# Optimization experiments

Hardware: AMD Instinct MI355X
Metric: run time of the kernel (lower is better)

The kernel has to match this reference:

```python
import jax, jax.numpy as jnp
import numpy as np

NUM_HEADS = 12
HEAD_DIM = 64
HIDDEN = 768
QMAX = 127.0  # 8-bit symmetric
DOMAIN_MIN, DOMAIN_MAX = -10.0, 0.0
NUM_INTERVALS = 12


def _build_pla_coeffs():
    xs = np.linspace(DOMAIN_MIN, DOMAIN_MAX, 1001)
    ys = np.exp(xs)
    intervals = np.linspace(DOMAIN_MIN, DOMAIN_MAX, NUM_INTERVALS + 1)
    ms, cs = [], []
    for i in range(NUM_INTERVALS):
        a, b = intervals[i], intervals[i + 1]
        mask = (xs >= a) & (xs <= b)
        m, c = np.polyfit(xs[mask], ys[mask], 1)
        ms.append(m)
        cs.append(c)
    return (jnp.asarray(ms, jnp.float32), jnp.asarray(cs, jnp.float32),
            jnp.asarray(intervals, jnp.float32))

COEFFS_M, COEFFS_C, INTERVALS = _build_pla_coeffs()


def quantize(x):
    # per-row (last-dim) abs-max symmetric 8-bit fake quant
    max_val = jnp.max(jnp.abs(x), axis=-1, keepdims=True)
    scale = max_val / QMAX
    scale = jnp.where(scale == 0, 1.0, scale)
    return jnp.clip(jnp.round(x / scale), -QMAX, QMAX) * scale


def to_fixed_point(x, bits=32, frac_bits=26):
    scale = 2.0 ** frac_bits
    lo = -2.0 ** (bits - 1)
    hi = 2.0 ** (bits - 1) - 1
    return jnp.clip(jnp.round(x * scale), lo, hi) / scale


def pla_exp(x):
    xc = jnp.clip(x, DOMAIN_MIN, DOMAIN_MAX)
    # sum(x >= intervals) - 1 == searchsorted(intervals, x, 'right') - 1
    idx = jnp.clip(jnp.searchsorted(INTERVALS, xc, side='right') - 1, 0, NUM_INTERVALS - 1)
    return COEFFS_M[idx] * xc + COEFFS_C[idx]


def pla_softmax(scores):
    shifted = scores - jnp.max(scores, axis=-1, keepdims=True)
    shifted_fx = to_fixed_point(shifted, 32, 26)
    exps = pla_exp(shifted_fx)
    sm = exps / (jnp.sum(exps, axis=-1, keepdims=True) + 1e-9)
    return quantize(sm)


def q_linear(x, W, b):
    # QuantizedLinear: quantize input and weight (per-row), fp bias
    return quantize(x) @ quantize(W).T + b


def split_heads(x):
    B, S, _ = x.shape
    return x.reshape(B, S, NUM_HEADS, HEAD_DIM).transpose(0, 2, 1, 3)  # bhsd


def mhsa(hidden_states, Wq, bq, Wk, bk, Wv, bv, Wo, bo):
    B, S, H = hidden_states.shape
    scale = HEAD_DIM ** -0.5
    q = split_heads(q_linear(hidden_states, Wq, bq))
    k = split_heads(q_linear(hidden_states, Wk, bk))
    v = split_heads(q_linear(hidden_states, Wv, bv))
    # per-row quantization makes tile-wise quant identical to full quant
    scores = jnp.einsum('bhqd,bhkd->bhqk', quantize(q), quantize(k)) * scale
    probs = pla_softmax(scores)
    ctx = jnp.einsum('bhqk,bhkd->bhqd', probs, quantize(v))
    ctx = ctx.transpose(0, 2, 1, 3).reshape(B, S, H)
    return q_linear(ctx, Wo, bo)


def setup_inputs() -> dict:
    key = jax.random.key(0)
    ks = jax.random.split(key, 9)
    B, S = 8, 512
    hs = jax.random.normal(ks[0], (B, S, HIDDEN), dtype=jnp.float32)
    def w(k):
        return jax.random.normal(k, (HIDDEN, HIDDEN), dtype=jnp.float32) * 0.02
    def b(k):
        return jax.random.normal(k, (HIDDEN,), dtype=jnp.float32) * 0.02
    return {
        'hidden_states': hs,
        'Wq': w(ks[1]), 'bq': b(ks[2]),
        'Wk': w(ks[3]), 'bk': b(ks[4]),
        'Wv': w(ks[5]), 'bv': b(ks[6]),
        'Wo': w(ks[7]), 'bo': b(ks[8]),
    }


def reference(hidden_states, Wq, bq, Wk, bk, Wv, bv, Wo, bo):
    return mhsa(hidden_states, Wq, bq, Wk, bk, Wv, bv, Wo, bo)
```

## Files before the change

### kernel.cpp

```cpp
#include <hip/hip_runtime.h>
#include <cmath>

#define R_TOT 4096
#define HID   768
#define NHEAD 12
#define HDIM  64
#define SEQ   512
#define BATCH 8

typedef int   v4i  __attribute__((ext_vector_type(4)));
typedef float v4f  __attribute__((ext_vector_type(4)));
typedef _Float16 half8 __attribute__((ext_vector_type(8)));
typedef _Float16 half4v __attribute__((ext_vector_type(4)));

struct PlaConsts { float m[12]; float c[12]; float b[13]; };

static PlaConsts build_pla() {
  PlaConsts pc;
  const int NPTS = 1001;
  static double xs[NPTS], ys[NPTS];
  const double step = 10.0 / 1000.0;
  for (int j = 0; j < NPTS; ++j) xs[j] = (double)j * step + (-10.0);
  xs[NPTS - 1] = 0.0;
  for (int j = 0; j < NPTS; ++j) ys[j] = std::exp(xs[j]);
  double bnd[13];
  const double step2 = 10.0 / 12.0;
  for (int k = 0; k < 13; ++k) bnd[k] = (double)k * step2 + (-10.0);
  bnd[12] = 0.0;
  for (int i = 0; i < 12; ++i) {
    const double a = bnd[i], bb = bnd[i + 1];
    double sx = 0, sy = 0; int n = 0;
    for (int j = 0; j < NPTS; ++j)
      if (xs[j] >= a && xs[j] <= bb) { sx += xs[j]; sy += ys[j]; ++n; }
    const double xm = sx / n, ym = sy / n;
    double sxx = 0, sxy = 0;
    for (int j = 0; j < NPTS; ++j)
      if (xs[j] >= a && xs[j] <= bb) {
        const double dx = xs[j] - xm;
        sxx += dx * dx; sxy += dx * (ys[j] - ym);
      }
    const double m = sxy / sxx;
    pc.m[i] = (float)m;
    pc.c[i] = (float)(ym - m * xm);
  }
  for (int k = 0; k < 13; ++k) pc.b[k] = (float)bnd[k];
  return pc;
}
static const PlaConsts g_pla = build_pla();

__device__ __forceinline__ void quant_row_body(const float* __restrict__ x,
                                               signed char* __restrict__ qrow,
                                               float* __restrict__ srow) {
  const float v0 = x[threadIdx.x];
  const float v1 = x[threadIdx.x + 256];
  const float v2 = x[threadIdx.x + 512];
  float m = fmaxf(fmaxf(fabsf(v0), fabsf(v1)), fabsf(v2));
  #pragma unroll
  for (int off = 32; off; off >>= 1) m = fmaxf(m, __shfl_xor(m, off));
  __shared__ float red[4];
  const int lane = threadIdx.x & 63, wv = threadIdx.x >> 6;
  if (lane == 0) red[wv] = m;
  __syncthreads();
  if (threadIdx.x == 0) {
    float mm = fmaxf(fmaxf(red[0], red[1]), fmaxf(red[2], red[3]));
    float s = mm / 127.0f;
    if (s == 0.f) s = 1.f;
    red[0] = s;
    *srow = s;
  }
  __syncthreads();
  const float s = red[0];
  qrow[threadIdx.x] =
      (signed char)(int)fminf(fmaxf(rintf(v0 / s), -127.f), 127.f);
  qrow[threadIdx.x + 256] =
      (signed char)(int)fminf(fmaxf(rintf(v1 / s), -127.f), 127.f);
  qrow[threadIdx.x + 512] =
      (signed char)(int)fminf(fmaxf(rintf(v2 / s), -127.f), 127.f);
}

__global__ __launch_bounds__(256)
void quant_rows(const float* __restrict__ src,
                signed char* __restrict__ qout, float* __restrict__ sout) {
  const int row = blockIdx.x;
  quant_row_body(src + (size_t)row * HID, qout + (size_t)row * HID, sout + row);
}

__global__ __launch_bounds__(256)
void quant_all(const float* hs, const float* w0, const float* w1,
               const float* w2, const float* w3,
               signed char* qx, float* sx,
               signed char* q0, signed char* q1, signed char* q2, signed char* q3,
               float* s0, float* s1, float* s2, float* s3) {
  const int bid = blockIdx.x;
  const float* src; signed char* qo; float* so; int row;
  if (bid < R_TOT)            { src = hs; qo = qx; so = sx; row = bid; }
  else if (bid < R_TOT + 768) { src = w0; qo = q0; so = s0; row = bid - R_TOT; }
  else if (bid < R_TOT + 1536){ src = w1; qo = q1; so = s1; row = bid - R_TOT - 768; }
  else if (bid < R_TOT + 2304){ src = w2; qo = q2; so = s2; row = bid - R_TOT - 1536; }
  else                        { src = w3; qo = q3; so = s3; row = bid - R_TOT - 2304; }
  quant_row_body(src + (size_t)row * HID, qo + (size_t)row * HID, so + row);
}

__device__ __forceinline__
void proj_body(int mode,
               const signed char* __restrict__ qx, const float* __restrict__ sx,
               const signed char* __restrict__ qw, const float* __restrict__ sw,
               const float* __restrict__ bias,
               signed char* __restrict__ qo, float* __restrict__ so,
               _Float16* __restrict__ vt, float* __restrict__ fo,
               signed char* Al, signed char* Bl) {
  const int tid = threadIdx.x;
  const int w = tid >> 6, lane = tid & 63;
  const int n = lane & 15, quad = lane >> 4;
  const int row0 = blockIdx.x * 128, col0 = blockIdx.y * 64;
  const int ar = tid >> 1, ac = (tid & 1) * 64;
  const int br = tid >> 2, bc = (tid & 3) * 32;
  v4i acc[2][4];
  #pragma unroll
  for (int s = 0; s < 2; ++s)
    #pragma unroll
    for (int j = 0; j < 4; ++j) acc[s][j] = (v4i){0, 0, 0, 0};
  for (int k0 = 0; k0 < HID; k0 += 128) {
    const signed char* ap = qx + (size_t)(row0 + ar) * HID + k0 + ac;
    const int4 a0 = *(const int4*)(ap);
    const int4 a1 = *(const int4*)(ap + 16);
    const int4 a2 = *(const int4*)(ap + 32);
    const int4 a3 = *(const int4*)(ap + 48);
    const signed char* bp = qw + (size_t)(col0 + br) * HID + k0 + bc;
    const int4 b0 = *(const int4*)(bp);
    const int4 b1 = *(const int4*)(bp + 16);
    if (k0) __syncthreads();
    *(int4*)&Al[ar * 144 + ac]      = a0;
    *(int4*)&Al[ar * 144 + ac + 16] = a1;
    *(int4*)&Al[ar * 144 + ac + 32] = a2;
    *(int4*)&Al[ar * 144 + ac + 48] = a3;
    *(int4*)&Bl[br * 144 + bc]      = b0;
    *(int4*)&Bl[br * 144 + bc + 16] = b1;
    __syncthreads();
    #pragma unroll
    for (int ks = 0; ks < 128; ks += 64) {
      const v4i af0 = *(const v4i*)&Al[(w * 16 + n) * 144 + ks + quad * 16];
      const v4i af1 = *(const v4i*)&Al[(64 + w * 16 + n) * 144 + ks + quad * 16];
      #pragma unroll
      for (int j = 0; j < 4; ++j) {
        const v4i bf = *(const v4i*)&Bl[(j * 16 + n) * 144 + ks + quad * 16];
        acc[0][j] = __builtin_amdgcn_mfma_i32_16x16x64_i8(af0, bf, acc[0][j], 0, 0, 0);
        acc[1][j] = __builtin_amdgcn_mfma_i32_16x16x64_i8(af1, bf, acc[1][j], 0, 0, 0);
      }
    }
  }
  float swc4[4], bc4[4];
  #pragma unroll
  for (int j = 0; j < 4; ++j) {
    swc4[j] = sw[col0 + j * 16 + n];
    bc4[j] = bias[col0 + j * 16 + n];
  }
  #pragma unroll
  for (int s = 0; s < 2; ++s) {
    const int mrow = s * 64 + w * 16 + quad * 4;
    float sxr[4];
    #pragma unroll
    for (int r = 0; r < 4; ++r) sxr[r] = sx[row0 + mrow + r];
    float vals[4][4];
    #pragma unroll
    for (int j = 0; j < 4; ++j)
      #pragma unroll
      for (int r = 0; r < 4; ++r)
        vals[j][r] = (float)acc[s][j][r] * (sxr[r] * swc4[j]) + bc4[j];
    if (mode == 1) {
      const int h = blockIdx.y;
      #pragma unroll
      for (int r = 0; r < 4; ++r) {
        float m = 0.f;
        #pragma unroll
        for (int j = 0; j < 4; ++j) m = fmaxf(m, fabsf(vals[j][r]));
        #pragma unroll
        for (int off = 1; off < 16; off <<= 1) m = fmaxf(m, __shfl_xor(m, off));
        float sq = m / 127.0f;
        if (sq == 0.f) sq = 1.f;
        const int grow = row0 + mrow + r;
        const int bidx = grow >> 9, sidx = grow & 511;
        const size_t rowidx = ((size_t)bidx * NHEAD + h) * SEQ + sidx;
        #pragma unroll
        for (int j = 0; j < 4; ++j) {
          float q = fminf(fmaxf(rintf(vals[j][r] / sq), -127.f), 127.f);
          qo[rowidx * HDIM + j * 16 + n] = (signed char)(int)q;
        }
        if (n == 0) so[rowidx] = sq;
      }
    } else if (mode == 2) {
      const int h = blockIdx.y;
      float srow[4];
      #pragma unroll
      for (int r = 0; r < 4; ++r) {
        float m = 0.f;
        #pragma unroll
        for (int j = 0; j < 4; ++j) m = fmaxf(m, fabsf(vals[j][r]));
        #pragma unroll
        for (int off = 1; off < 16; off <<= 1) m = fmaxf(m, __shfl_xor(m, off));
        float sq = m / 127.0f;
        if (sq == 0.f) sq = 1.f;
        srow[r] = sq;
      }
      const int grow0 = row0 + mrow;
      const int bidx = grow0 >> 9, sidx = grow0 & 511;
      const int kb = sidx >> 5, ko = sidx & 31;
      const size_t hbv = (size_t)bidx * NHEAD + h;
      #pragma unroll
      for (int j = 0; j < 4; ++j) {
        half4v hv;
        #pragma unroll
        for (int r = 0; r < 4; ++r) {
          float q = fminf(fmaxf(rintf(vals[j][r] / srow[r]), -127.f), 127.f);
          hv[r] = (_Float16)(q * srow[r]);
        }
        *(half4v*)(vt + ((hbv * 16 + kb) * 64 + j * 16 + n) * 32 + ko) = hv;
      }
    } else {
      #pragma unroll
      for (int r = 0; r < 4; ++r) {
        const size_t base = (size_t)(row0 + mrow + r) * HID + col0;
        #pragma unroll
        for (int j = 0; j < 4; ++j)
          fo[base + j * 16 + n] = vals[j][r];
      }
    }
  }
}

__global__ __launch_bounds__(256)
void proj_qkv(const signed char* __restrict__ qx, const float* __restrict__ sx,
              const signed char* qwq, const float* swq, const float* bq,
              signed char* qqd, float* qqs,
              const signed char* qwk, const float* swk, const float* bk,
              signed char* qkd, float* qks,
              const signed char* qwv, const float* swv, const float* bv,
              _Float16* vt2) {
  __shared__ __align__(16) signed char Al[128 * 144];
  __shared__ __align__(16) signed char Bl[64 * 144];
  if (blockIdx.z == 0)
    proj_body(1, qx, sx, qwq, swq, bq, qqd, qqs, nullptr, nullptr, Al, Bl);
  else if (blockIdx.z == 1)
    proj_body(1, qx, sx, qwk, swk, bk, qkd, qks, nullptr, nullptr, Al, Bl);
  else
    proj_body(2, qx, sx, qwv, swv, bv, nullptr, nullptr, vt2, nullptr, Al, Bl);
}

__global__ __launch_bounds__(256)
void proj_out(const signed char* __restrict__ qx, const float* __restrict__ sx,
              const signed char* qw, const float* sw, const float* bias,
              float* fo) {
  __shared__ __align__(16) signed char Al[128 * 144];
  __shared__ __align__(16) signed char Bl[64 * 144];
  proj_body(0, qx, sx, qw, sw, bias, nullptr, nullptr, nullptr, fo, Al, Bl);
}

__device__ __forceinline__
void softmax_exp_tile(float (&s)[8][4], float mx26, const float4* __restrict__ pt4,
                      float& sum_out, float& amax_out) {
  float sum = 0.f, amax = 0.f;
  #pragma unroll
  for (int t = 0; t < 8; ++t) {
    #pragma unroll
    for (int r = 0; r < 4; ++r) {
      float sh = s[t][r] - mx26;
      sh = fmaxf(sh, -671088640.0f);
      const float tq = rintf(sh);
      const float xc = tq * 1.4901161193847656e-08f;
      int g = (int)((xc + 10.0f) * 1.2f);
      g = g > 11 ? 11 : g;
      float4 E = pt4[g];
      int gn = g + ((xc >= E.y) ? 1 : 0) - ((xc < E.x) ? 1 : 0);
      gn = gn < 0 ? 0 : (gn > 11 ? 11 : gn);
      if (gn != g) E = pt4[gn];
      const float e = __fadd_rn(__fmul_rn(E.z, xc), E.w);
      s[t][r] = e;
      sum += e;
      amax = fmaxf(amax, fabsf(e));
    }
  }
  sum += __shfl_xor(sum, 16);
  sum += __shfl_xor(sum, 32);
  amax = fmaxf(amax, __shfl_xor(amax, 16));
  amax = fmaxf(amax, __shfl_xor(amax, 32));
  sum_out = sum; amax_out = amax;
}

__device__ __forceinline__
void quant_pack_tile(const float (&s)[8][4], float t127,
                     _Float16* __restrict__ phtrow, int w, int quad) {
  #pragma unroll
  for (int t = 0; t < 8; ++t) {
    half4v hq;
    #pragma unroll
    for (int r = 0; r < 4; ++r) {
      const float qf = fminf(fmaxf(rintf(s[t][r] * t127), -127.f), 127.f);
      hq[r] = (_Float16)qf;
    }
    *(half4v*)&phtrow[(t * 4 + w) * 16 + quad * 4] = hq;
  }
}

__device__ __forceinline__
v4f pv_tile(const _Float16* __restrict__ vbase, const _Float16* __restrict__ prow) {
  v4f acc = {0.f, 0.f, 0.f, 0.f};
  #pragma unroll
  for (int kt = 0; kt < 16; ++kt) {
    const half8 bf = *(const half8*)(vbase + kt * 2048);
    acc = __builtin_amdgcn_mfma_f32_16x16x32_f16(*(const half8*)(prow + kt * 32), bf, acc, 0, 0, 0);
  }
  return acc;
}

#define PSTR 520
__global__ __launch_bounds__(256)
void attn_kernel(const signed char* __restrict__ qq, const float* __restrict__ qss,
                 const signed char* __restrict__ qk, const float* __restrict__ kss,
                 const _Float16* __restrict__ vt2,
                 float* __restrict__ ctx, const PlaConsts pc) {
  __shared__ __align__(16) _Float16 PhT[2][16 * PSTR];
  __shared__ __align__(16) float red_max[2][16][4];
  __shared__ __align__(16) float red_sum[2][16][4];
  __shared__ __align__(16) float red_amax[2][16][4];
  __shared__ float psa[2][16];
  __shared__ __align__(16) float4 pt4[12];

  const int tid = threadIdx.x;
  const int q0 = blockIdx.x * 32;
  const int hh = blockIdx.y, bz = blockIdx.z;
  const size_t hb = (size_t)bz * NHEAD + hh;
  const signed char* qqh = qq + (hb * SEQ + q0) * HDIM;
  const signed char* qkh = qk + hb * SEQ * HDIM;
  const float* ksp = kss + hb * SEQ;

  if (tid < 12)
    pt4[tid] = make_float4(pc.b[tid], pc.b[tid + 1], pc.m[tid], pc.c[tid]);

  const int w = tid >> 6, lane = tid & 63;
  const int n = lane & 15, quad = lane >> 4;

  float s26[2][8][4];
  {
    const v4i qf0 = *(const v4i*)(qqh + (size_t)n * HDIM + quad * 16);
    const v4i qf1 = *(const v4i*)(qqh + (size_t)(16 + n) * HDIM + quad * 16);
    const float qs0 = (qss[hb * SEQ + q0 + n] * 0.125f) * 67108864.0f;
    const float qs1 = (qss[hb * SEQ + q0 + 16 + n] * 0.125f) * 67108864.0f;
    float vmax0 = -3.0e38f, vmax1 = -3.0e38f;
    #pragma unroll
    for (int t = 0; t < 8; ++t) {
      const int kc0 = (t * 4 + w) * 16;
      const v4i kfrag = *(const v4i*)(qkh + (size_t)(kc0 + n) * HDIM + quad * 16);
      const float4 ks4 = *(const float4*)(ksp + kc0 + quad * 4);
      v4i zero = {};
      const v4i a0 = __builtin_amdgcn_mfma_i32_16x16x64_i8(kfrag, qf0, zero, 0, 0, 0);
      const v4i a1 = __builtin_amdgcn_mfma_i32_16x16x64_i8(kfrag, qf1, zero, 0, 0, 0);
      const float ks[4] = {ks4.x, ks4.y, ks4.z, ks4.w};
      #pragma unroll
      for (int r = 0; r < 4; ++r) {
        const float v0 = (float)a0[r] * (qs0 * ks[r]);
        const float v1 = (float)a1[r] * (qs1 * ks[r]);
        s26[0][t][r] = v0; vmax0 = fmaxf(vmax0, v0);
        s26[1][t][r] = v1; vmax1 = fmaxf(vmax1, v1);
      }
    }
    vmax0 = fmaxf(vmax0, __shfl_xor(vmax0, 16));
    vmax0 = fmaxf(vmax0, __shfl_xor(vmax0, 32));
    vmax1 = fmaxf(vmax1, __shfl_xor(vmax1, 16));
    vmax1 = fmaxf(vmax1, __shfl_xor(vmax1, 32));
    if (quad == 0) { red_max[0][n][w] = vmax0; red_max[1][n][w] = vmax1; }
  }
  __syncthreads();

  {
    const float4 rm = *(const float4*)&red_max[0][n][0];
    const float mx26 = fmaxf(fmaxf(rm.x, rm.y), fmaxf(rm.z, rm.w));
    float sum, amax;
    softmax_exp_tile(s26[0], mx26, pt4, sum, amax);
    if (quad == 0) { red_sum[0][n][w] = sum; red_amax[0][n][w] = amax; }
  }
  __syncthreads();

  {
    const float4 rs = *(const float4*)&red_sum[0][n][0];
    const float4 ra = *(const float4*)&red_amax[0][n][0];
    float denom = (rs.x + rs.y) + (rs.z + rs.w);
    denom = __fadd_rn(denom, 1e-9f);
    const float rden = 1.0f / denom;
    const float am = fmaxf(fmaxf(ra.x, ra.y), fmaxf(ra.z, ra.w));
    float ps = (am * rden) / 127.0f;
    if (ps == 0.f) ps = 1.f;
    if (w == 0 && quad == 0) psa[0][n] = ps;
    const float t127 = 127.0f / am;
    quant_pack_tile(s26[0], t127, &PhT[0][n * PSTR], w, quad);

    const float4 rm = *(const float4*)&red_max[1][n][0];
    const float mx26 = fmaxf(fmaxf(rm.x, rm.y), fmaxf(rm.z, rm.w));
    float sum, amax;
    softmax_exp_tile(s26[1], mx26, pt4, sum, amax);
    if (quad == 0) { red_sum[1][n][w] = sum; red_amax[1][n][w] = amax; }
  }
  __syncthreads();

  const _Float16* vbase = vt2 + ((size_t)hb * 16 * 64 + (w * 16 + n)) * 32 + quad * 8;

  {
    const v4f acc0 = pv_tile(vbase, &PhT[0][n * PSTR + quad * 8]);

    const float4 rs = *(const float4*)&red_sum[1][n][0];
    const float4 ra = *(const float4*)&red_amax[1][n][0];
    float denom = (rs.x + rs.y) + (rs.z + rs.w);
    denom = __fadd_rn(denom, 1e-9f);
    const float rden = 1.0f / denom;
    const float am = fmaxf(fmaxf(ra.x, ra.y), fmaxf(ra.z, ra.w));
    float ps = (am * rden) / 127.0f;
    if (ps == 0.f) ps = 1.f;
    if (w == 0 && quad == 0) psa[1][n] = ps;
    const float t127 = 127.0f / am;
    quant_pack_tile(s26[1], t127, &PhT[1][n * PSTR], w, quad);

    #pragma unroll
    for (int r = 0; r < 4; ++r) {
      const int row = quad * 4 + r;
      ctx[((size_t)bz * SEQ + q0 + row) * HID + (size_t)hh * HDIM + w * 16 + n] =
          acc0[r] * psa[0][row];
    }
  }
  __syncthreads();

  {
    const v4f acc1 = pv_tile(vbase, &PhT[1][n * PSTR + quad * 8]);
    #pragma unroll
    for (int r = 0; r < 4; ++r) {
      const int row = quad * 4 + r;
      ctx[((size_t)bz * SEQ + q0 + 16 + row) * HID + (size_t)hh * HDIM + w * 16 + n] =
          acc1[r] * psa[1][row];
    }
  }
}

extern "C" void kernel_launch(void* const* d_in, const int* in_sizes, int n_in,
                              void* d_out, int out_size, void* d_ws, size_t ws_size,
                              hipStream_t stream) {
  (void)in_sizes; (void)n_in; (void)out_size; (void)ws_size;
  const float* hs = (const float*)d_in[0];
  const float* Wq = (const float*)d_in[1];
  const float* bq = (const float*)d_in[2];
  const float* Wk = (const float*)d_in[3];
  const float* bk = (const float*)d_in[4];
  const float* Wv = (const float*)d_in[5];
  const float* bv = (const float*)d_in[6];
  const float* Wo = (const float*)d_in[7];
  const float* bo = (const float*)d_in[8];
  float* out = (float*)d_out;

  char* ws = (char*)d_ws;
  size_t off = 0;
  auto alloc = [&](size_t bytes) -> char* {
    char* p = ws + off;
    off += (bytes + 255) & ~(size_t)255;
    return p;
  };
  signed char* qx  = (signed char*)alloc((size_t)R_TOT * HID);
  float*       sx  = (float*)alloc((size_t)R_TOT * 4);
  signed char* qwq = (signed char*)alloc((size_t)HID * HID);
  signed char* qwk = (signed char*)alloc((size_t)HID * HID);
  signed char* qwv = (signed char*)alloc((size_t)HID * HID);
  signed char* qwo = (signed char*)alloc((size_t)HID * HID);
  float*       swq = (float*)alloc((size_t)HID * 4);
  float*       swk = (float*)alloc((size_t)HID * 4);
  float*       swv = (float*)alloc((size_t)HID * 4);
  float*       swo = (float*)alloc((size_t)HID * 4);
  signed char* qqd = (signed char*)alloc((size_t)R_TOT * HID);
  float*       qqs = (float*)alloc((size_t)BATCH * NHEAD * SEQ * 4);
  signed char* qkd = (signed char*)alloc((size_t)R_TOT * HID);
  float*       qks = (float*)alloc((size_t)BATCH * NHEAD * SEQ * 4);
  float*       ctx = (float*)alloc((size_t)R_TOT * HID * 4);
  _Float16*    vt2 = (_Float16*)alloc((size_t)BATCH * NHEAD * HDIM * SEQ * 2);
  signed char* qc  = qx;
  float*       scs = sx;

  quant_all<<<R_TOT + 4 * HID, 256, 0, stream>>>(
      hs, Wq, Wk, Wv, Wo, qx, sx,
      qwq, qwk, qwv, qwo, swq, swk, swv, swo);

  proj_qkv<<<dim3(R_TOT / 128, HID / 64, 3), 256, 0, stream>>>(
      qx, sx, qwq, swq, bq, qqd, qqs,
      qwk, swk, bk, qkd, qks,
      qwv, swv, bv, vt2);

  attn_kernel<<<dim3(SEQ / 32, NHEAD, BATCH), 256, 0, stream>>>(
      qqd, qqs, qkd, qks, vt2, ctx, g_pla);

  quant_rows<<<R_TOT, 256, 0, stream>>>(ctx, qc, scs);
  proj_out<<<dim3(R_TOT / 128, HID / 64), 256, 0, stream>>>(
      qc, scs, qwo, swo, bo, out);
}
```

Baseline: 153.7 us.

## Load projection GEMM tiles directly into LDS with XOR-swizzled layout

Replaces the register-staged global loads and LDS stores in the int8 projection GEMM with global_load_lds direct-to-LDS transfers. The padded 144-byte row stride becomes an unpadded 128-byte stride with a 16-byte-chunk XOR swizzle, which avoids LDS bank conflicts when fragments are read for the MFMA. This removes VGPR staging and shrinks LDS use. The tradeoff is reliance on the direct-load builtin's per-lane address layout being correct, and the loop still has no double buffering, so load latency is not overlapped with compute.

```diff
diff --git a/kernel.cpp b/kernel.cpp
--- a/kernel.cpp
+++ b/kernel.cpp
@@ -12,6 +12,12 @@
 typedef float v4f  __attribute__((ext_vector_type(4)));
 typedef _Float16 half8 __attribute__((ext_vector_type(8)));
 typedef _Float16 half4v __attribute__((ext_vector_type(4)));
+
+__device__ __forceinline__ void gl_lds16(const signed char* g, signed char* l) {
+  __builtin_amdgcn_global_load_lds(
+      (const __attribute__((address_space(1))) void*)g,
+      (__attribute__((address_space(3))) void*)l, 16, 0, 0);
+}
 
 struct PlaConsts { float m[12]; float c[12]; float b[13]; };
 
@@ -113,37 +119,37 @@
   const int w = tid >> 6, lane = tid & 63;
   const int n = lane & 15, quad = lane >> 4;
   const int row0 = blockIdx.x * 128, col0 = blockIdx.y * 64;
-  const int ar = tid >> 1, ac = (tid & 1) * 64;
-  const int br = tid >> 2, bc = (tid & 3) * 32;
+  const int lr = lane >> 3;
+  const int lc = lane & 7;
+  const int cg = lc ^ lr;
   v4i acc[2][4];
   #pragma unroll
   for (int s = 0; s < 2; ++s)
     #pragma unroll
     for (int j = 0; j < 4; ++j) acc[s][j] = (v4i){0, 0, 0, 0};
   for (int k0 = 0; k0 < HID; k0 += 128) {
-    const signed char* ap = qx + (size_t)(row0 + ar) * HID + k0 + ac;
-    const int4 a0 = *(const int4*)(ap);
-    const int4 a1 = *(const int4*)(ap + 16);
-    const int4 a2 = *(const int4*)(ap + 32);
-    const int4 a3 = *(const int4*)(ap + 48);
-    const signed char* bp = qw + (size_t)(col0 + br) * HID + k0 + bc;
-    const int4 b0 = *(const int4*)(bp);
-    const int4 b1 = *(const int4*)(bp + 16);
     if (k0) __syncthreads();
-    *(int4*)&Al[ar * 144 + ac]      = a0;
-    *(int4*)&Al[ar * 144 + ac + 16] = a1;
-    *(int4*)&Al[ar * 144 + ac + 32] = a2;
-    *(int4*)&Al[ar * 144 + ac + 48] = a3;
-    *(int4*)&Bl[br * 144 + bc]      = b0;
-    *(int4*)&Bl[br * 144 + bc + 16] = b1;
+    #pragma unroll
+    for (int m = 0; m < 4; ++m) {
+      const int ci = w * 4 + m;
+      gl_lds16(qx + (size_t)(row0 + ci * 8 + lr) * HID + k0 + cg * 16,
+               Al + ci * 1024);
+    }
+    #pragma unroll
+    for (int m = 0; m < 2; ++m) {
+      const int ci = w * 2 + m;
+      gl_lds16(qw + (size_t)(col0 + ci * 8 + lr) * HID + k0 + cg * 16,
+               Bl + ci * 1024);
+    }
     __syncthreads();
     #pragma unroll
-    for (int ks = 0; ks < 128; ks += 64) {
-      const v4i af0 = *(const v4i*)&Al[(w * 16 + n) * 144 + ks + quad * 16];
-      const v4i af1 = *(const v4i*)&Al[(64 + w * 16 + n) * 144 + ks + quad * 16];
+    for (int ks4 = 0; ks4 < 8; ks4 += 4) {
+      const int sw16 = ((quad + ks4) ^ (n & 7)) * 16;
+      const v4i af0 = *(const v4i*)&Al[(w * 16 + n) * 128 + sw16];
+      const v4i af1 = *(const v4i*)&Al[(64 + w * 16 + n) * 128 + sw16];
       #pragma unroll
       for (int j = 0; j < 4; ++j) {
-        const v4i bf = *(const v4i*)&Bl[(j * 16 + n) * 144 + ks + quad * 16];
+        const v4i bf = *(const v4i*)&Bl[(j * 16 + n) * 128 + sw16];
         acc[0][j] = __builtin_amdgcn_mfma_i32_16x16x64_i8(af0, bf, acc[0][j], 0, 0, 0);
         acc[1][j] = __builtin_amdgcn_mfma_i32_16x16x64_i8(af1, bf, acc[1][j], 0, 0, 0);
       }
@@ -236,8 +242,8 @@
               signed char* qkd, float* qks,
               const signed char* qwv, const float* swv, const float* bv,
               _Float16* vt2) {
-  __shared__ __align__(16) signed char Al[128 * 144];
-  __shared__ __align__(16) signed char Bl[64 * 144];
+  __shared__ __align__(16) signed char Al[128 * 128];
+  __shared__ __align__(16) signed char Bl[64 * 128];
   if (blockIdx.z == 0)
     proj_body(1, qx, sx, qwq, swq, bq, qqd, qqs, nullptr, nullptr, Al, Bl);
   else if (blockIdx.z == 1)
@@ -250,8 +256,8 @@
 void proj_out(const signed char* __restrict__ qx, const float* __restrict__ sx,
               const signed char* qw, const float* sw, const float* bias,
               float* fo) {
-  __shared__ __align__(16) signed char Al[128 * 144];
-  __shared__ __align__(16) signed char Bl[64 * 144];
+  __shared__ __align__(16) signed char Al[128 * 128];
+  __shared__ __align__(16) signed char Bl[64 * 128];
   proj_body(0, qx, sx, qw, sw, bias, nullptr, nullptr, nullptr, fo, Al, Bl);
 }
 
```

Measured after the change: 149.8 us. 1.03x faster.
